# Kernel optimization log

Measured on AMD Instinct MI355X. Metric: run time of the kernel, lower is better.

Reference implementation:

```python
import jax, jax.numpy as jnp
import numpy as np
from jax import lax

EPS = 0.1
MAX_ITER = 100
THRESH = 0.01
N = 4  # number of prompt ensembles


def _l2norm(x, axis):
    return x / jnp.linalg.norm(x, axis=axis, keepdims=True)


def sinkhorn(K, u, v, max_iter=MAX_ITER, thresh=THRESH):
    # K: [B, M, N], u: [B, M], v: [B, N]. Matches torch loop with early exit
    # on mean(|r - r0|) < thresh, done on-device via lax.while_loop.
    dt = K.dtype
    r0 = jnp.ones_like(u)
    c0 = jnp.ones_like(v)

    def cond(state):
        _, _, i, err = state
        return jnp.logical_and(i < max_iter, err >= thresh)

    def body(state):
        r, c, i, _ = state
        r_new = u / jnp.einsum('bmn,bn->bm', K, c)
        c_new = v / jnp.einsum('bmn,bm->bn', K, r_new)
        err = jnp.mean(jnp.abs(r_new - r))
        return (r_new, c_new, i + 1, err)

    r, c, _, _ = lax.while_loop(cond, body, (r0, c0, jnp.int32(0), jnp.asarray(jnp.inf, dt)))
    # T = outer(r, c) * K
    return r[:, :, None] * c[:, None, :] * K


def setup_inputs() -> dict:
    key = jax.random.key(0)
    k1, k2, k3 = jax.random.split(key, 3)
    M, b, d = 196, 32, 512
    n_cls = 1000
    return {
        'image_features': jax.random.normal(k1, (M, b, d), dtype=jnp.float32),
        'image_feature_pool': jax.random.normal(k2, (b, d), dtype=jnp.float32),
        'text_features': jax.random.normal(k3, (N * n_cls, d), dtype=jnp.float32),
        'logit_scale': jnp.asarray(np.log(1.0 / 0.07), dtype=jnp.float32),
    }


def reference(image_features, image_feature_pool, text_features, logit_scale):
    M, b, d = image_features.shape
    n_cls = text_features.shape[0] // N

    tf = text_features.reshape(N, n_cls, d)
    text_feature_pool = tf.mean(axis=0)

    imf = _l2norm(image_features, axis=2)          # [M, b, d]
    img_pool = _l2norm(image_feature_pool, axis=1)  # [b, d]
    tfn = _l2norm(tf, axis=2)                       # [N, n_cls, d]
    txt_pool = _l2norm(text_feature_pool, axis=1)   # [n_cls, d]

    # sim: [M, N, b, n_cls] -> [M, N, b*n_cls] -> [B, M, N]
    sim = jnp.einsum('mbd,ncd->mnbc', imf, tfn)
    sim = sim.reshape(M, N, b * n_cls).transpose(2, 0, 1)
    wdist = 1.0 - sim

    B = b * n_cls
    xx = jnp.full((B, M), 1.0 / M, dtype=sim.dtype)
    yy = jnp.full((B, N), 1.0 / N, dtype=sim.dtype)

    # torch.no_grad() around Sinkhorn -> stop gradients into the iteration
    K = jnp.exp(-lax.stop_gradient(wdist) / EPS)
    T = sinkhorn(K, xx, yy)

    sim_op = jnp.sum(T * sim, axis=(1, 2)).reshape(b, n_cls)

    ls = jnp.exp(logit_scale)
    logits = ls * (img_pool @ txt_pool.T)
    logits2 = 0.5 * (ls * sim_op) + 0.5 * logits
    return logits2
```

## Files before the change

kernel.cpp:

```cpp
#include <hip/hip_runtime.h>
#include <hip/hip_bf16.h>

#define MB 6272
#define NC 4000
#define DD 512
#define NCLS 1000
#define NB 32000
#define NITER 6
#define SK_STRIDE 68

typedef __attribute__((ext_vector_type(8))) short short8;
typedef __attribute__((ext_vector_type(4))) float f32x4;
typedef __attribute__((ext_vector_type(2))) float f32x2;

__device__ __forceinline__ float bflo(unsigned u) { return __builtin_bit_cast(float, u << 16); }
__device__ __forceinline__ float bfhi(unsigned u) { return __builtin_bit_cast(float, u & 0xFFFF0000u); }
__device__ __forceinline__ float frcp(float x) { return __builtin_amdgcn_rcpf(x); }

__device__ __forceinline__ unsigned short f2bf(float x) {
  unsigned u = __builtin_bit_cast(unsigned, x);
  u += 0x7FFFu + ((u >> 16) & 1u);
  return (unsigned short)(u >> 16);
}

__device__ __forceinline__ bool is_fp32_mode(const void* lsp) {
  const unsigned short u = *(const unsigned short*)lsp;
  const float v = __builtin_bit_cast(float, (unsigned)u << 16);
  return !(v > 2.55f && v < 2.77f);
}

__device__ __forceinline__ void gl_lds16(const unsigned short* g, unsigned short* l) {
  __builtin_amdgcn_global_load_lds(
      (const __attribute__((address_space(1))) void*)g,
      (__attribute__((address_space(3))) void*)l, 16, 0, 0);
}

__global__ __launch_bounds__(256) void prep(const void* __restrict__ imgf,
                                            const void* __restrict__ imgp,
                                            const void* __restrict__ txtf,
                                            const void* __restrict__ lsp,
                                            float* __restrict__ rnAT, float* __restrict__ rnB,
                                            float* __restrict__ imgpool,
                                            float* __restrict__ txtpool,
                                            unsigned short* __restrict__ Ab,
                                            unsigned short* __restrict__ Bb) {
  const bool f32 = is_fp32_mode(lsp);
  const int w = threadIdx.x >> 6;
  const int lane = threadIdx.x & 63;
  const int row = blockIdx.x * 4 + w;
  const int d0 = lane * 8;

  float v[8];
  auto load8f = [&](const void* base, int srow) {
    if (f32) {
      const float4 a = *reinterpret_cast<const float4*>((const float*)base + (size_t)srow * DD + d0);
      const float4 b = *reinterpret_cast<const float4*>((const float*)base + (size_t)srow * DD + d0 + 4);
      v[0] = a.x; v[1] = a.y; v[2] = a.z; v[3] = a.w;
      v[4] = b.x; v[5] = b.y; v[6] = b.z; v[7] = b.w;
    } else {
      const uint4 u = *reinterpret_cast<const uint4*>((const unsigned short*)base + (size_t)srow * DD + d0);
      v[0] = bflo(u.x); v[1] = bfhi(u.x); v[2] = bflo(u.y); v[3] = bfhi(u.y);
      v[4] = bflo(u.z); v[5] = bfhi(u.z); v[6] = bflo(u.w); v[7] = bfhi(u.w);
    }
  };

  int mode;
  unsigned short* dst16 = nullptr;
  float* dstf = nullptr;
  int outidx = 0;
  if (row < MB) {
    load8f(imgf, row); mode = 0; dst16 = Ab + (size_t)row * DD + d0;
    outidx = (row & 31) * 208 + (row >> 5);
  } else if (row < MB + NC) {
    const int j = row - MB;
    load8f(txtf, (j & 3) * NCLS + (j >> 2)); mode = 1;
    dst16 = Bb + (size_t)j * DD + d0; outidx = j;
  } else if (row < MB + NC + 32) {
    const int b = row - MB - NC;
    load8f(imgp, b); mode = 2; dstf = imgpool + (size_t)b * DD + d0;
  } else {
    const int cc = row - (MB + NC + 32);
    float acc8[8] = {0, 0, 0, 0, 0, 0, 0, 0};
#pragma unroll
    for (int n = 0; n < 4; ++n) {
      load8f(txtf, n * NCLS + cc);
#pragma unroll
      for (int i = 0; i < 8; ++i) acc8[i] += v[i];
    }
#pragma unroll
    for (int i = 0; i < 8; ++i) v[i] = acc8[i] * 0.25f;
    mode = 3; dstf = txtpool + (size_t)cc * DD + d0;
  }

  float ss = 0.f;
#pragma unroll
  for (int i = 0; i < 8; ++i) ss += v[i] * v[i];
#pragma unroll
  for (int off = 1; off < 64; off <<= 1) ss += __shfl_xor(ss, off);
  const float rn = rsqrtf(ss);

  if (mode <= 1) {
    union { uint4 u; unsigned short h[8]; } r;
#pragma unroll
    for (int i = 0; i < 8; ++i) r.h[i] = f2bf(v[i]);
    *reinterpret_cast<uint4*>(dst16) = r.u;
    if (lane == 0) (mode == 0 ? rnAT : rnB)[outidx] = rn;
  } else {
    float4 a, b;
    a.x = v[0] * rn; a.y = v[1] * rn; a.z = v[2] * rn; a.w = v[3] * rn;
    b.x = v[4] * rn; b.y = v[5] * rn; b.z = v[6] * rn; b.w = v[7] * rn;
    *reinterpret_cast<float4*>(dstf) = a;
    *reinterpret_cast<float4*>(dstf + 4) = b;
  }
}

__global__ __launch_bounds__(256, 3) void gemm_sink(const unsigned short* __restrict__ Ab,
                                                    const unsigned short* __restrict__ Bb,
                                                    const float* __restrict__ rnAT,
                                                    const float* __restrict__ rnB,
                                                    const float* __restrict__ imgpool,
                                                    const float* __restrict__ txtpool,
                                                    const void* __restrict__ lsp,
                                                    void* __restrict__ out) {
  __shared__ unsigned short shm[17408];
  __shared__ float rnAs[208];

  const int t = threadIdx.x;
  const int lane = t & 63;
  const int w = t >> 6;
  const int b = blockIdx.x;
  const int y = blockIdx.y;
  const int quad = lane >> 4, l16 = lane & 15;

  const int mbase = (w == 0) ? 0 : (3 * w + 1);
  const int nmt = (w == 0) ? 4 : 3;

  if (t < 208) rnAs[t] = rnAT[b * 208 + t];

  const unsigned short* asrc[3];
#pragma unroll
  for (int r = 0; r < 3; ++r) {
    const int g = r * 256 + t;
    const int rr = g >> 2;
    const int seg = g & 3;
    const int sg = (seg ^ (rr & 3)) * 8;
    asrc[r] = Ab + (size_t)(rr * 32 + b) * DD + sg;
  }
  const int xrr = 192 + (lane >> 2);
  const int xseg = lane & 3;
  const int xsg = (xseg ^ (xrr & 3)) * 8;
  const int xarow = xrr < 196 ? xrr : 195;
  const unsigned short* axsrc = Ab + (size_t)(xarow * 32 + b) * DD + xsg;
  const unsigned short* bsrc;
  {
    const int rr = t >> 2;
    const int seg = t & 3;
    const int sg = (seg ^ (rr & 3)) * 8;
    const int jg0 = y * 64 + rr;
    const int jg = jg0 < NC ? jg0 : NC - 1;
    bsrc = Bb + (size_t)jg * DD + sg;
  }

  f32x4 acc[4][4];
#pragma unroll
  for (int i = 0; i < 4; ++i)
#pragma unroll
    for (int jt = 0; jt < 4; ++jt) acc[i][jt] = (f32x4)0.f;

  unsigned short* const buf0 = shm;
  unsigned short* const buf1 = shm + 8704;

  auto stage = [&](unsigned short* buf, int koff) {
#pragma unroll
    for (int r = 0; r < 3; ++r)
      gl_lds16(asrc[r] + koff, buf + (size_t)(r * 256 + w * 64) * 8);
    if (w == 0) gl_lds16(axsrc + koff, buf + (size_t)768 * 8);
    gl_lds16(bsrc + koff, buf + 6656 + (size_t)(w * 64) * 8);
  };

  auto compute = [&](const unsigned short* cb) {
    const unsigned short* Bsx = cb + 6656;
    short8 bfr[4];
#pragma unroll
    for (int jt = 0; jt < 4; ++jt) {
      const int rwb = jt * 16 + l16;
      bfr[jt] = *reinterpret_cast<const short8*>(&Bsx[rwb * 32 + (quad ^ (rwb & 3)) * 8]);
    }
    __builtin_amdgcn_s_setprio(1);
#pragma unroll
    for (int i = 0; i < 4; ++i) {
      if (i < nmt) {
        const int rw = (mbase + i) * 16 + l16;
        const short8 af = *reinterpret_cast<const short8*>(&cb[rw * 32 + (quad ^ (rw & 3)) * 8]);
#pragma unroll
        for (int jt = 0; jt < 4; ++jt)
          acc[i][jt] = __builtin_amdgcn_mfma_f32_16x16x32_bf16(af, bfr[jt], acc[i][jt], 0, 0, 0);
      }
    }
    __builtin_amdgcn_s_setprio(0);
  };

  stage(buf0, 0);
  asm volatile("s_waitcnt vmcnt(0)" ::: "memory");
  __syncthreads();

#pragma unroll 1
  for (int kt = 0; kt < 16; kt += 2) {
    stage(buf1, (kt + 1) * 32);
    compute(buf0);
    asm volatile("s_waitcnt vmcnt(0)" ::: "memory");
    __builtin_amdgcn_s_barrier();
    if (kt < 14) stage(buf0, (kt + 2) * 32);
    compute(buf1);
    asm volatile("s_waitcnt vmcnt(0)" ::: "memory");
    __builtin_amdgcn_s_barrier();
  }

  {
    float rbv[4];
#pragma unroll
    for (int jt = 0; jt < 4; ++jt) {
      const int jg = y * 64 + jt * 16 + l16;
      rbv[jt] = jg < NC ? rnB[jg] : 1.0f;
    }
#pragma unroll
    for (int i = 0; i < 4; ++i) {
      if (i < nmt) {
#pragma unroll
        for (int jt = 0; jt < 4; ++jt) {
          const int jl = jt * 16 + l16;
#pragma unroll
          for (int reg = 0; reg < 4; ++reg) {
            const int m = (mbase + i) * 16 + quad * 4 + reg;
            if (m < 196) {
              const float sim = acc[i][jt][reg] * rnAs[m] * rbv[jt];
              shm[m * SK_STRIDE + jl] = f2bf(__expf(10.f * sim - 10.f));
            }
          }
        }
      }
    }
  }
  __syncthreads();

  const int pl = lane >> 4;
  const int sub = lane & 15;
  const int mstart = sub < 4 ? sub * 13 : 52 + (sub - 4) * 12;
  const int pcol = (w * 4 + pl) * 4;

  uint2 kk[13];
#pragma unroll
  for (int i = 0; i < 13; ++i) {
    const int m = mstart + i;
    const int mc = m < 196 ? m : 195;
    kk[i] = *reinterpret_cast<const uint2*>(&shm[mc * SK_STRIDE + pcol]);
  }

  f32x2 cA = {1.f, 1.f}, cB = {1.f, 1.f};
  for (int it = 0; it < NITER - 1; ++it) {
    f32x2 SA = {0.f, 0.f}, SB = {0.f, 0.f};
#pragma unroll
    for (int i = 0; i < 13; ++i) {
      if (i < 12 || sub < 4) {
        f32x2 kA = {bflo(kk[i].x), bfhi(kk[i].x)};
        f32x2 kB = {bflo(kk[i].y), bfhi(kk[i].y)};
        const f32x2 pr = kA * cA + kB * cB;
        const float rv = (1.0f / 196.0f) * frcp(pr.x + pr.y);
        const f32x2 rvv = {rv, rv};
        SA += kA * rvv;
        SB += kB * rvv;
      }
    }
    SA.x += __shfl_xor(SA.x, 1); SA.x += __shfl_xor(SA.x, 2); SA.x += __shfl_xor(SA.x, 4); SA.x += __shfl_xor(SA.x, 8);
    SA.y += __shfl_xor(SA.y, 1); SA.y += __shfl_xor(SA.y, 2); SA.y += __shfl_xor(SA.y, 4); SA.y += __shfl_xor(SA.y, 8);
    SB.x += __shfl_xor(SB.x, 1); SB.x += __shfl_xor(SB.x, 2); SB.x += __shfl_xor(SB.x, 4); SB.x += __shfl_xor(SB.x, 8);
    SB.y += __shfl_xor(SB.y, 1); SB.y += __shfl_xor(SB.y, 2); SB.y += __shfl_xor(SB.y, 4); SB.y += __shfl_xor(SB.y, 8);
    cA.x = 0.25f * frcp(SA.x); cA.y = 0.25f * frcp(SA.y);
    cB.x = 0.25f * frcp(SB.x); cB.y = 0.25f * frcp(SB.y);
  }

  f32x2 SA = {0.f, 0.f}, SB = {0.f, 0.f}, WA = {0.f, 0.f}, WB = {0.f, 0.f};
#pragma unroll
  for (int i = 0; i < 13; ++i) {
    if (i < 12 || sub < 4) {
      f32x2 kA = {bflo(kk[i].x), bfhi(kk[i].x)};
      f32x2 kB = {bflo(kk[i].y), bfhi(kk[i].y)};
      const f32x2 pr = kA * cA + kB * cB;
      const float rv = (1.0f / 196.0f) * frcp(pr.x + pr.y);
      const f32x2 rvv = {rv, rv};
      const f32x2 tA = kA * rvv, tB = kB * rvv;
      SA += tA; SB += tB;
      const f32x2 lgA = {__logf(kA.x), __logf(kA.y)};
      const f32x2 lgB = {__logf(kB.x), __logf(kB.y)};
      const f32x2 one = {1.f, 1.f}, tenth = {0.1f, 0.1f};
      WA += tA * (one + tenth * lgA);
      WB += tB * (one + tenth * lgB);
    }
  }
  SA.x += __shfl_xor(SA.x, 1); SA.x += __shfl_xor(SA.x, 2); SA.x += __shfl_xor(SA.x, 4); SA.x += __shfl_xor(SA.x, 8);
  SA.y += __shfl_xor(SA.y, 1); SA.y += __shfl_xor(SA.y, 2); SA.y += __shfl_xor(SA.y, 4); SA.y += __shfl_xor(SA.y, 8);
  SB.x += __shfl_xor(SB.x, 1); SB.x += __shfl_xor(SB.x, 2); SB.x += __shfl_xor(SB.x, 4); SB.x += __shfl_xor(SB.x, 8);
  SB.y += __shfl_xor(SB.y, 1); SB.y += __shfl_xor(SB.y, 2); SB.y += __shfl_xor(SB.y, 4); SB.y += __shfl_xor(SB.y, 8);
  WA.x += __shfl_xor(WA.x, 1); WA.x += __shfl_xor(WA.x, 2); WA.x += __shfl_xor(WA.x, 4); WA.x += __shfl_xor(WA.x, 8);
  WA.y += __shfl_xor(WA.y, 1); WA.y += __shfl_xor(WA.y, 2); WA.y += __shfl_xor(WA.y, 4); WA.y += __shfl_xor(WA.y, 8);
  WB.x += __shfl_xor(WB.x, 1); WB.x += __shfl_xor(WB.x, 2); WB.x += __shfl_xor(WB.x, 4); WB.x += __shfl_xor(WB.x, 8);
  WB.y += __shfl_xor(WB.y, 1); WB.y += __shfl_xor(WB.y, 2); WB.y += __shfl_xor(WB.y, 4); WB.y += __shfl_xor(WB.y, 8);
  const float simop = (0.25f * frcp(SA.x)) * WA.x + (0.25f * frcp(SA.y)) * WA.y +
                      (0.25f * frcp(SB.x)) * WB.x + (0.25f * frcp(SB.y)) * WB.y;

  const int cg = y * 16 + (w * 4 + pl);
  const int cgc = cg < NCLS ? cg : NCLS - 1;
  const float4* ip4 = reinterpret_cast<const float4*>(imgpool + (size_t)b * DD);
  const float4* tp4 = reinterpret_cast<const float4*>(txtpool + (size_t)cgc * DD);
  float dot = 0.f;
#pragma unroll
  for (int i = 0; i < 8; ++i) {
    const float4 a = ip4[sub * 8 + i];
    const float4 v = tp4[sub * 8 + i];
    dot += (a.x * v.x + a.y * v.y) + (a.z * v.z + a.w * v.w);
  }
  dot += __shfl_xor(dot, 1); dot += __shfl_xor(dot, 2); dot += __shfl_xor(dot, 4); dot += __shfl_xor(dot, 8);

  if (sub == 0 && cg < NCLS) {
    const bool f32 = is_fp32_mode(lsp);
    const float lsv = f32 ? *(const float*)lsp : bflo(*(const unsigned short*)lsp);
    const float val = 0.5f * __expf(lsv) * (simop + dot);
    const int p = b * NCLS + cg;
    if (f32) ((float*)out)[p] = val;
    else ((unsigned short*)out)[p] = f2bf(val);
  }
}

extern "C" void kernel_launch(void* const* d_in, const int* in_sizes, int n_in,
                              void* d_out, int out_size, void* d_ws, size_t ws_size,
                              hipStream_t stream) {
  const void* imgf = d_in[0];
  const void* imgp = d_in[1];
  const void* txtf = d_in[2];
  const void* lsp  = d_in[3];

  const size_t need = (size_t)32 * 208 * 4 + NC * 4 + 32 * DD * 4 + NCLS * DD * 4 +
                      (size_t)MB * DD * 2 + (size_t)NC * DD * 2;
  const bool ok = (n_in == 4) && in_sizes[0] == MB * DD && in_sizes[1] == 32 * DD &&
                  in_sizes[2] == NC * DD && in_sizes[3] == 1 && out_size == NB &&
                  ws_size >= need;
  if (!ok) return;

  char* w = (char*)d_ws;
  float* rnAT = (float*)w;                 w += (size_t)32 * 208 * 4;
  float* rnB = (float*)w;                  w += NC * 4;
  float* imgpool = (float*)w;              w += 32 * DD * 4;
  float* txtpool = (float*)w;              w += NCLS * DD * 4;
  unsigned short* Ab = (unsigned short*)w; w += (size_t)MB * DD * 2;
  unsigned short* Bb = (unsigned short*)w; w += (size_t)NC * DD * 2;

  prep<<<dim3(2826), dim3(256), 0, stream>>>(imgf, imgp, txtf, lsp, rnAT, rnB,
                                             imgpool, txtpool, Ab, Bb);
  gemm_sink<<<dim3(32, 63), dim3(256), 0, stream>>>(Ab, Bb, rnAT, rnB, imgpool,
                                                    txtpool, lsp, d_out);
}
```

Before: 140.8 us.

## Load A fragments directly into registers and triple-buffer B in LDS

The GEMM main loop stops staging the A tile through LDS. Each wave now prefetches its own A fragments straight from global memory into double-buffered registers. Only the B tile goes through LDS, now in a three-slot ring with one barrier per k-step and a partial vmcnt wait, so the next loads overlap the current MFMAs. This removes LDS write/read traffic for A and one barrier per step. In exchange it raises register pressure and relies on scattered 16-byte global loads of A rows being served from cache.

Result: slower. 164.6 us (+16.9%).

```diff
diff --git a/kernel.cpp b/kernel.cpp
--- a/kernel.cpp
+++ b/kernel.cpp
@@ -122,7 +122,7 @@
                                                     const float* __restrict__ txtpool,
                                                     const void* __restrict__ lsp,
                                                     void* __restrict__ out) {
-  __shared__ unsigned short shm[17408];
+  __shared__ unsigned short shm[196 * SK_STRIDE];
   __shared__ float rnAs[208];
 
   const int t = threadIdx.x;
@@ -137,20 +137,13 @@
 
   if (t < 208) rnAs[t] = rnAT[b * 208 + t];
 
-  const unsigned short* asrc[3];
-#pragma unroll
-  for (int r = 0; r < 3; ++r) {
-    const int g = r * 256 + t;
-    const int rr = g >> 2;
-    const int seg = g & 3;
-    const int sg = (seg ^ (rr & 3)) * 8;
-    asrc[r] = Ab + (size_t)(rr * 32 + b) * DD + sg;
-  }
-  const int xrr = 192 + (lane >> 2);
-  const int xseg = lane & 3;
-  const int xsg = (xseg ^ (xrr & 3)) * 8;
-  const int xarow = xrr < 196 ? xrr : 195;
-  const unsigned short* axsrc = Ab + (size_t)(xarow * 32 + b) * DD + xsg;
+  const unsigned short* aptr[4];
+#pragma unroll
+  for (int i = 0; i < 4; ++i) {
+    const int mrow = (mbase + i) * 16 + l16;
+    const int arow = mrow < 196 ? mrow : 195;
+    aptr[i] = Ab + (size_t)(arow * 32 + b) * DD + quad * 8;
+  }
   const unsigned short* bsrc;
   {
     const int rr = t >> 2;
@@ -167,54 +160,60 @@
 #pragma unroll
     for (int jt = 0; jt < 4; ++jt) acc[i][jt] = (f32x4)0.f;
 
-  unsigned short* const buf0 = shm;
-  unsigned short* const buf1 = shm + 8704;
-
-  auto stage = [&](unsigned short* buf, int koff) {
-#pragma unroll
-    for (int r = 0; r < 3; ++r)
-      gl_lds16(asrc[r] + koff, buf + (size_t)(r * 256 + w * 64) * 8);
-    if (w == 0) gl_lds16(axsrc + koff, buf + (size_t)768 * 8);
-    gl_lds16(bsrc + koff, buf + 6656 + (size_t)(w * 64) * 8);
+  short8 a0[4], a1[4];
+
+  auto stageB = [&](unsigned short* buf, int koff) {
+    gl_lds16(bsrc + koff, buf + (size_t)(w * 64) * 8);
   };
-
-  auto compute = [&](const unsigned short* cb) {
-    const unsigned short* Bsx = cb + 6656;
+  auto prefA = [&](short8* areg, int koff) {
+#pragma unroll
+    for (int i = 0; i < 4; ++i)
+      if (i < nmt)
+        areg[i] = *reinterpret_cast<const short8*>(aptr[i] + koff);
+  };
+  auto compute = [&](const unsigned short* bb, const short8* areg) {
     short8 bfr[4];
 #pragma unroll
     for (int jt = 0; jt < 4; ++jt) {
       const int rwb = jt * 16 + l16;
-      bfr[jt] = *reinterpret_cast<const short8*>(&Bsx[rwb * 32 + (quad ^ (rwb & 3)) * 8]);
+      bfr[jt] = *reinterpret_cast<const short8*>(&bb[rwb * 32 + (quad ^ (rwb & 3)) * 8]);
     }
     __builtin_amdgcn_s_setprio(1);
 #pragma unroll
     for (int i = 0; i < 4; ++i) {
       if (i < nmt) {
-        const int rw = (mbase + i) * 16 + l16;
-        const short8 af = *reinterpret_cast<const short8*>(&cb[rw * 32 + (quad ^ (rw & 3)) * 8]);
 #pragma unroll
         for (int jt = 0; jt < 4; ++jt)
-          acc[i][jt] = __builtin_amdgcn_mfma_f32_16x16x32_bf16(af, bfr[jt], acc[i][jt], 0, 0, 0);
+          acc[i][jt] = __builtin_amdgcn_mfma_f32_16x16x32_bf16(areg[i], bfr[jt], acc[i][jt], 0, 0, 0);
       }
     }
     __builtin_amdgcn_s_setprio(0);
   };
 
-  stage(buf0, 0);
+  stageB(shm, 0);
+  prefA(a0, 0);
   asm volatile("s_waitcnt vmcnt(0)" ::: "memory");
   __syncthreads();
 
-#pragma unroll 1
-  for (int kt = 0; kt < 16; kt += 2) {
-    stage(buf1, (kt + 1) * 32);
-    compute(buf0);
-    asm volatile("s_waitcnt vmcnt(0)" ::: "memory");
+  int sc = 0;
+#pragma unroll 2
+  for (int k = 0; k < 16; ++k) {
+    const int sn = (sc == 2) ? 0 : sc + 1;
+    if (k < 15) {
+      stageB(shm + sn * 2048, (k + 1) * 32);
+      prefA((k & 1) ? a0 : a1, (k + 1) * 32);
+      __builtin_amdgcn_sched_barrier(0);
+      asm volatile("s_waitcnt vmcnt(5)" ::: "memory");
+      __builtin_amdgcn_sched_barrier(0);
+    } else {
+      asm volatile("s_waitcnt vmcnt(0)" ::: "memory");
+      __builtin_amdgcn_sched_barrier(0);
+    }
     __builtin_amdgcn_s_barrier();
-    if (kt < 14) stage(buf0, (kt + 2) * 32);
-    compute(buf1);
-    asm volatile("s_waitcnt vmcnt(0)" ::: "memory");
-    __builtin_amdgcn_s_barrier();
-  }
+    compute(shm + sc * 2048, (k & 1) ? a1 : a0);
+    sc = sn;
+  }
+  __syncthreads();
 
   {
     float rbv[4];
```
